# Kernel optimization log

Measured on AMD Instinct MI355X. Metric: run time of the kernel, lower is better.

## Reference

```python
import jax, jax.numpy as jnp
import numpy as np

N_NODES = 50000
N_EDGES = 400000
N_EDGE_SCALARS = 16   # 16x0e block
N_NODE_SCALARS = 64   # 64x0e node attrs
HEADS = 16            # max multiplicity
HEAD_DIM = 32
HID = 64              # mlp_latent_dimensions = [64, 64]
EDGE_DIM = 144        # 16*(1+3+5)
# (start, end, mul, ir.dim) for 16x0e + 16x1o + 16x2e
BLOCKS = [(0, 16, 16, 1), (16, 64, 16, 3), (64, 144, 16, 5)]
ISQRTD = 1.0 / float(np.sqrt(HEAD_DIM))


def _mlp(x, w1, b1, w2, b2, w3, b3):
    # ScalarMLPFunction: Linear -> SiLU -> Linear -> SiLU -> Linear
    h = jax.nn.silu(x @ w1 + b1)
    h = jax.nn.silu(h @ w2 + b2)
    return h @ w3 + b3


def setup_inputs() -> dict:
    key = jax.random.key(0)
    ks = jax.random.split(key, 16)
    def w(k, shape):
        fan_in = shape[0]
        return (jax.random.normal(k, shape, dtype=jnp.float32) / np.sqrt(fan_in)).astype(jnp.float32)
    out_dim = HEADS * HEAD_DIM
    return {
        "edge_index": jax.random.randint(ks[0], (2, N_EDGES), 0, N_NODES, dtype=jnp.int32),
        "edge_feat": jax.random.normal(ks[1], (N_EDGES, EDGE_DIM), dtype=jnp.float32),
        "node_attrs": jax.random.normal(ks[2], (N_NODES, N_NODE_SCALARS), dtype=jnp.float32),
        # node_attr_to_query MLP params
        "q_w1": w(ks[3], (N_NODE_SCALARS, HID)), "q_b1": jnp.zeros((HID,), jnp.float32),
        "q_w2": w(ks[4], (HID, HID)),            "q_b2": jnp.zeros((HID,), jnp.float32),
        "q_w3": w(ks[5], (HID, out_dim)),        "q_b3": jnp.zeros((out_dim,), jnp.float32),
        # edge_feat_to_key MLP params
        "k_w1": w(ks[6], (N_EDGE_SCALARS, HID)), "k_b1": jnp.zeros((HID,), jnp.float32),
        "k_w2": w(ks[7], (HID, HID)),            "k_b2": jnp.zeros((HID,), jnp.float32),
        "k_w3": w(ks[8], (HID, out_dim)),        "k_b3": jnp.zeros((out_dim,), jnp.float32),
    }


def reference(edge_index, edge_feat, node_attrs,
              q_w1, q_b1, q_w2, q_b2, q_w3, q_b3,
              k_w1, k_b1, k_w2, k_b2, k_w3, k_b3):
    edge_center = edge_index[0]  # [E]

    # gather node scalars to edges, then small MLPs -> Q, K per edge
    Q = _mlp(node_attrs[edge_center], q_w1, q_b1, q_w2, q_b2, q_w3, q_b3)
    Q = Q.reshape(-1, HEADS, HEAD_DIM)
    edge_scalars = edge_feat[:, :N_EDGE_SCALARS]
    K = _mlp(edge_scalars, k_w1, k_b1, k_w2, k_b2, k_w3, k_b3)
    K = K.reshape(-1, HEADS, HEAD_DIM)

    # per-edge, per-head logits
    W = jnp.einsum('ehd,ehd->eh', Q, K) * ISQRTD  # [E, H]

    # scatter-softmax over edges sharing the same center node
    seg_max = jax.ops.segment_max(W, edge_center, num_segments=N_NODES)  # [N, H]
    seg_max = jnp.where(jnp.isfinite(seg_max), seg_max, 0.0)
    ex = jnp.exp(W - seg_max[edge_center])
    denom = jax.ops.segment_sum(ex, edge_center, num_segments=N_NODES)
    attn = ex / denom[edge_center]  # [E, H]

    # reweight each irreps block by per-head attention (head h <-> multiplicity channel)
    E = edge_feat.shape[0]
    weighted = []
    for start, end, mul, dim in BLOCKS:
        blk = edge_feat[:, start:end].reshape(E, mul, dim) * attn[:, :mul, None]
        weighted.append(blk.reshape(E, mul * dim))
    w_edge = jnp.concatenate(weighted, axis=-1)  # [E, EDGE_DIM]

    # scatter-sum edges into center nodes
    return jax.ops.segment_sum(w_edge, edge_center, num_segments=N_NODES)  # [N, EDGE_DIM]
```

## Files before the change

### kernel.cpp

```cpp
#include <hip/hip_runtime.h>
#include <hip/hip_bf16.h>

constexpr int N_NODES  = 50000;
constexpr int N_EDGES  = 400000;
constexpr int EDGE_DIM = 144;
constexpr int HEADS    = 16;
constexpr int HEAD_DIM = 32;
constexpr int OUTD     = 512;
constexpr int HID      = 64;
constexpr int NES      = 16;
constexpr int NNS      = 64;
constexpr int SCAN_B   = 512;
constexpr int NSB      = (N_NODES + SCAN_B - 1) / SCAN_B;
constexpr int NPB_A    = 64;
#define ISQRTD 0.17677669529663687f

__device__ __forceinline__ float silu_f(float x) {
    return x / (1.0f + __expf(-x));
}

__device__ __forceinline__ unsigned fenc(float f) {
    unsigned u = __float_as_uint(f);
    return (u & 0x80000000u) ? ~u : (u | 0x80000000u);
}
__device__ __forceinline__ float fdec(unsigned m) {
    unsigned u = (m & 0x80000000u) ? (m ^ 0x80000000u) : ~m;
    return __uint_as_float(u);
}

__device__ __forceinline__ int headOf(int col) {
    return (col < 16) ? col : ((col < 64) ? (col - 16) / 3 : (col - 64) / 5);
}

__device__ __forceinline__ void storeQ(float* p, float v) { *p = v; }
__device__ __forceinline__ void storeQ(__hip_bfloat16* p, float v) { *p = __float2bfloat16(v); }
__device__ __forceinline__ float loadQ(const float* p) { return *p; }
__device__ __forceinline__ float loadQ(const __hip_bfloat16* p) { return __bfloat162float(*p); }

__global__ __launch_bounds__(256) void prep_kernel(
    const float* __restrict__ w1, const float* __restrict__ w2,
    float* __restrict__ w1T, float* __restrict__ w2T) {
    int t = blockIdx.x * 256 + threadIdx.x;
    if (t < NES * HID) {
        int i = t / HID, j = t % HID;
        w1T[j * NES + i] = w1[t];
    }
    if (t < HID * HID) {
        int i = t / HID, j = t % HID;
        w2T[j * HID + i] = w2[t];
    }
}

__global__ __launch_bounds__(256) void mbuild_kernel(
    const float* __restrict__ qw3, const float* __restrict__ qb3,
    const float* __restrict__ kw3, const float* __restrict__ kb3,
    float* __restrict__ M, float* __restrict__ C0,
    float* __restrict__ Mb, float* __restrict__ c1) {
    const int b = blockIdx.x, t = threadIdx.x;
    if (b < 256) {
        const int o  = b * 256 + t;
        const int hl = o & 3, j = (o >> 2) & 63, i = (o >> 8) & 63, hg = o >> 14;
        const int h  = hg * 4 + hl;
        const float* ka = kw3 + (size_t)i * OUTD + h * HEAD_DIM;
        const float* qa = qw3 + (size_t)j * OUTD + h * HEAD_DIM;
        float s = 0.f;
        #pragma unroll
        for (int d = 0; d < HEAD_DIM; ++d) s += ka[d] * qa[d];
        M[o] = s;
    } else if (b < 260) {
        const int o  = (b - 256) * 256 + t;
        const int hl = o & 3, i = (o >> 2) & 63, hg = o >> 8;
        const int h  = hg * 4 + hl;
        float s = 0.f;
        #pragma unroll
        for (int d = 0; d < HEAD_DIM; ++d)
            s += kw3[(size_t)i * OUTD + h * HEAD_DIM + d] * qb3[h * HEAD_DIM + d];
        C0[o] = s;
    } else if (b < 264) {
        const int o = (b - 260) * 256 + t;
        const int h = o >> 6, j = o & 63;
        float s = 0.f;
        #pragma unroll
        for (int d = 0; d < HEAD_DIM; ++d)
            s += kb3[h * HEAD_DIM + d] * qw3[(size_t)j * OUTD + h * HEAD_DIM + d];
        Mb[o] = s;
    } else {
        if (t < HEADS) {
            float s = 0.f;
            #pragma unroll
            for (int d = 0; d < HEAD_DIM; ++d)
                s += kb3[t * HEAD_DIM + d] * qb3[t * HEAD_DIM + d];
            c1[t] = s;
        }
    }
}

__global__ __launch_bounds__(256) void h2q_kernel(
    const float* __restrict__ node_attrs,
    const float* __restrict__ w1, const float* __restrict__ b1,
    const float* __restrict__ w2, const float* __restrict__ b2,
    const float* __restrict__ Mb, const float* __restrict__ c1,
    float* __restrict__ h2buf, float* __restrict__ Sn) {
    __shared__ float xs[4][NNS];
    __shared__ float h1s[4][HID];
    __shared__ float h2s[4][HID];
    __shared__ float Mbs[HEADS][65];
    __shared__ float c1s[HEADS];
    const int t = threadIdx.x, wid = t >> 6, lane = t & 63;
    for (int o = t; o < HEADS * HID; o += 256) Mbs[o >> 6][o & 63] = Mb[o];
    if (t < HEADS) c1s[t] = c1[t];

    const int n = blockIdx.x * 4 + wid;
    const bool act = n < N_NODES;
    xs[wid][lane] = act ? node_attrs[(size_t)n * NNS + lane] : 0.0f;
    __syncthreads();

    float a = b1[lane];
    #pragma unroll
    for (int i = 0; i < NNS; ++i) a += xs[wid][i] * w1[i * HID + lane];
    h1s[wid][lane] = silu_f(a);
    __syncthreads();

    float a2 = b2[lane];
    #pragma unroll
    for (int i = 0; i < HID; ++i) a2 += h1s[wid][i] * w2[i * HID + lane];
    const float h2v = silu_f(a2);
    h2s[wid][lane] = h2v;
    if (act) h2buf[(size_t)n * HID + lane] = h2v;
    __syncthreads();

    const int h = lane & 15, q = lane >> 4;
    float s = 0.f;
    #pragma unroll
    for (int jj = 0; jj < 16; ++jj) s += h2s[wid][q * 16 + jj] * Mbs[h][q * 16 + jj];
    s += __shfl_xor(s, 16);
    s += __shfl_xor(s, 32);
    if (act && lane < HEADS) Sn[(size_t)n * HEADS + lane] = s + c1s[lane];
}

__global__ __launch_bounds__(256) void papply_kernel(
    const float* __restrict__ h2buf, const float* __restrict__ M,
    const float* __restrict__ C0, float* __restrict__ Pn) {
    const int t  = threadIdx.x;
    const int hg = blockIdx.y;

    float Mreg[HID];
    const float* msrc = M + (size_t)hg * 16384 + (t >> 2) * 256 + (t & 3);
    #pragma unroll
    for (int j = 0; j < HID; ++j) Mreg[j] = msrc[j * 4];
    const float c0 = C0[hg * 256 + t];

    __shared__ float h2s[4][HID];
    const int n0 = blockIdx.x * NPB_A;
    #pragma unroll 1
    for (int s4 = 0; s4 < NPB_A / 4; ++s4) {
        const int nb = n0 + s4 * 4;
        const int nl = nb + (t >> 6);
        const float v = (nl < N_NODES) ? h2buf[(size_t)nl * HID + (t & 63)] : 0.f;
        __syncthreads();
        h2s[t >> 6][t & 63] = v;
        __syncthreads();
        #pragma unroll 1
        for (int mm = 0; mm < 4; ++mm) {
            const int n = nb + mm;
            if (n >= N_NODES) break;
            float acc0 = c0, acc1 = 0.f;
            #pragma unroll
            for (int j = 0; j < HID; j += 2) {
                acc0 += h2s[mm][j]     * Mreg[j];
                acc1 += h2s[mm][j + 1] * Mreg[j + 1];
            }
            Pn[(size_t)n * 1024 + hg * 256 + t] = acc0 + acc1;
        }
    }
}

__global__ __launch_bounds__(256) void zero_counts_kernel(int* __restrict__ counts) {
    int t = blockIdx.x * 256 + threadIdx.x;
    if (t < N_NODES) counts[t] = 0;
}
__global__ __launch_bounds__(256) void hist_kernel(const int* __restrict__ center,
                                                   int* __restrict__ counts) {
    int e = blockIdx.x * 256 + threadIdx.x;
    if (e < N_EDGES) atomicAdd(&counts[center[e]], 1);
}
__global__ __launch_bounds__(SCAN_B) void scan1_kernel(
    const int* __restrict__ counts, int* __restrict__ incl, int* __restrict__ blockSums) {
    __shared__ int sm[SCAN_B];
    const int gid = blockIdx.x * SCAN_B + threadIdx.x;
    sm[threadIdx.x] = (gid < N_NODES) ? counts[gid] : 0;
    __syncthreads();
    #pragma unroll 1
    for (int off = 1; off < SCAN_B; off <<= 1) {
        int t = (threadIdx.x >= off) ? sm[threadIdx.x - off] : 0;
        __syncthreads();
        sm[threadIdx.x] += t;
        __syncthreads();
    }
    if (gid < N_NODES) incl[gid] = sm[threadIdx.x];
    if (threadIdx.x == SCAN_B - 1) blockSums[blockIdx.x] = sm[threadIdx.x];
}
__global__ void scan2_kernel(int* __restrict__ blockSums) {
    if (threadIdx.x == 0 && blockIdx.x == 0) {
        int run = 0;
        for (int i = 0; i < NSB; ++i) { int t = blockSums[i]; blockSums[i] = run; run += t; }
    }
}
__global__ __launch_bounds__(SCAN_B) void scan3_kernel(
    const int* __restrict__ counts, const int* __restrict__ incl,
    const int* __restrict__ blockSums, int* __restrict__ rowStart,
    int* __restrict__ cursor) {
    const int gid = blockIdx.x * SCAN_B + threadIdx.x;
    if (gid < N_NODES) {
        const int excl = incl[gid] - counts[gid] + blockSums[blockIdx.x];
        rowStart[gid] = excl;
        cursor[gid]   = excl;
    }
    if (gid == 0) rowStart[N_NODES] = N_EDGES;
}
__global__ __launch_bounds__(256) void fill_kernel(const int* __restrict__ center,
                                                   int* __restrict__ cursor,
                                                   int* __restrict__ edgeList,
                                                   int* __restrict__ nodeOf) {
    int e = blockIdx.x * 256 + threadIdx.x;
    if (e < N_EDGES) {
        const int c = center[e];
        int pos = atomicAdd(&cursor[c], 1);
        edgeList[pos] = e;
        nodeOf[pos]   = c;
    }
}

__global__ __launch_bounds__(256, 2) void wpass5_kernel(
    const int* __restrict__ edgeList, const int* __restrict__ nodeOf,
    const float* __restrict__ edge_feat,
    const float* __restrict__ w1T, const float* __restrict__ b1,
    const float* __restrict__ w2T, const float* __restrict__ b2,
    const float* __restrict__ Pn, const float* __restrict__ Sn,
    float* __restrict__ Wbuf) {
    const int p = blockIdx.x * 256 + threadIdx.x;
    if (p >= N_EDGES) return;
    const int e = edgeList[p];
    const int c = nodeOf[p];

    float x[NES];
    const float4* ef4 = reinterpret_cast<const float4*>(edge_feat + (size_t)e * EDGE_DIM);
    #pragma unroll
    for (int i = 0; i < NES / 4; ++i) {
        float4 t = ef4[i];
        x[4*i+0] = t.x; x[4*i+1] = t.y; x[4*i+2] = t.z; x[4*i+3] = t.w;
    }

    float h1[HID];
    #pragma unroll
    for (int j = 0; j < HID; ++j) {
        float a0 = 0.f, a1 = 0.f, a2 = 0.f, a3 = 0.f;
        const float* wr = w1T + j * NES;
        #pragma unroll
        for (int i = 0; i < NES; i += 4) {
            a0 += x[i + 0] * wr[i + 0];
            a1 += x[i + 1] * wr[i + 1];
            a2 += x[i + 2] * wr[i + 2];
            a3 += x[i + 3] * wr[i + 3];
        }
        h1[j] = silu_f(b1[j] + ((a0 + a1) + (a2 + a3)));
    }

    float wacc[HEADS];
    {
        const float4* s4 = (const float4*)(Sn + (size_t)c * HEADS);
        #pragma unroll
        for (int k = 0; k < 4; ++k) {
            float4 v = s4[k];
            wacc[4*k+0] = v.x; wacc[4*k+1] = v.y; wacc[4*k+2] = v.z; wacc[4*k+3] = v.w;
        }
    }

    const float* prow = Pn + (size_t)c * 1024;
    #pragma unroll 2
    for (int j = 0; j < HID; ++j) {
        float a0 = 0.f, a1 = 0.f, a2 = 0.f, a3 = 0.f;
        const float* wr = w2T + j * HID;
        #pragma unroll
        for (int i = 0; i < HID; i += 4) {
            a0 += h1[i + 0] * wr[i + 0];
            a1 += h1[i + 1] * wr[i + 1];
            a2 += h1[i + 2] * wr[i + 2];
            a3 += h1[i + 3] * wr[i + 3];
        }
        const float h2 = silu_f(b2[j] + ((a0 + a1) + (a2 + a3)));
        #pragma unroll
        for (int hg = 0; hg < 4; ++hg) {
            const float4 pv = *(const float4*)(prow + hg * 256 + j * 4);
            wacc[hg*4+0] += h2 * pv.x;
            wacc[hg*4+1] += h2 * pv.y;
            wacc[hg*4+2] += h2 * pv.z;
            wacc[hg*4+3] += h2 * pv.w;
        }
    }

    float4* wrow = (float4*)(Wbuf + (size_t)p * HEADS);
    #pragma unroll
    for (int k = 0; k < 4; ++k) {
        wrow[k] = make_float4(wacc[4*k+0] * ISQRTD, wacc[4*k+1] * ISQRTD,
                              wacc[4*k+2] * ISQRTD, wacc[4*k+3] * ISQRTD);
    }
}

__global__ __launch_bounds__(256) void gather4_kernel(
    const int* __restrict__ rowStart, const int* __restrict__ edgeList,
    const float* __restrict__ edge_feat, const float* __restrict__ Wbuf,
    float* __restrict__ out) {
    const int wid  = threadIdx.x >> 6;
    const int lane = threadIdx.x & 63;
    const int n = blockIdx.x * 4 + wid;
    if (n >= N_NODES) return;
    const int rs = rowStart[n];
    const int d  = rowStart[n + 1] - rs;

    const int c0 = lane, c1 = lane + 64, c2 = lane + 128;
    const int h0 = headOf(c0);
    const int h1 = headOf(c1);
    const int h2 = (c2 < EDGE_DIM) ? headOf(c2) : 0;
    const bool has2 = (c2 < EDGE_DIM);

    float acc0 = 0.f, acc1 = 0.f, acc2 = 0.f;
    if (d > 0) {
        const int hh  = lane & 15;
        const int sub = lane >> 4;
        float m = -3.0e38f;
        for (int i = sub; i < d; i += 4)
            m = fmaxf(m, Wbuf[(size_t)(rs + i) * HEADS + hh]);
        m = fmaxf(m, __shfl_xor(m, 16));
        m = fmaxf(m, __shfl_xor(m, 32));
        float s = 0.f;
        for (int i = sub; i < d; i += 4)
            s += __expf(Wbuf[(size_t)(rs + i) * HEADS + hh] - m);
        s += __shfl_xor(s, 16);
        s += __shfl_xor(s, 32);
        const float rden = 1.0f / s;

        int i = 0;
        for (; i + 4 <= d; i += 4) {
            const int eA = edgeList[rs + i + 0];
            const int eB = edgeList[rs + i + 1];
            const int eC = edgeList[rs + i + 2];
            const int eD = edgeList[rs + i + 3];
            const float wA = Wbuf[(size_t)(rs + i + 0) * HEADS + hh];
            const float wB = Wbuf[(size_t)(rs + i + 1) * HEADS + hh];
            const float wC = Wbuf[(size_t)(rs + i + 2) * HEADS + hh];
            const float wD = Wbuf[(size_t)(rs + i + 3) * HEADS + hh];
            const float* frA = edge_feat + (size_t)eA * EDGE_DIM;
            const float* frB = edge_feat + (size_t)eB * EDGE_DIM;
            const float* frC = edge_feat + (size_t)eC * EDGE_DIM;
            const float* frD = edge_feat + (size_t)eD * EDGE_DIM;
            const float fA0 = frA[c0], fB0 = frB[c0], fC0 = frC[c0], fD0 = frD[c0];
            const float fA1 = frA[c1], fB1 = frB[c1], fC1 = frC[c1], fD1 = frD[c1];
            const float fA2 = has2 ? frA[c2] : 0.f;
            const float fB2 = has2 ? frB[c2] : 0.f;
            const float fC2 = has2 ? frC[c2] : 0.f;
            const float fD2 = has2 ? frD[c2] : 0.f;

            const float aLA = __expf(wA - m) * rden;
            const float aLB = __expf(wB - m) * rden;
            const float aLC = __expf(wC - m) * rden;
            const float aLD = __expf(wD - m) * rden;
            const float aA0 = __shfl(aLA, h0), aB0 = __shfl(aLB, h0);
            const float aC0 = __shfl(aLC, h0), aD0 = __shfl(aLD, h0);
            const float aA1 = __shfl(aLA, h1), aB1 = __shfl(aLB, h1);
            const float aC1 = __shfl(aLC, h1), aD1 = __shfl(aLD, h1);
            const float aA2 = __shfl(aLA, h2), aB2 = __shfl(aLB, h2);
            const float aC2 = __shfl(aLC, h2), aD2 = __shfl(aLD, h2);

            acc0 += (fA0 * aA0 + fB0 * aB0) + (fC0 * aC0 + fD0 * aD0);
            acc1 += (fA1 * aA1 + fB1 * aB1) + (fC1 * aC1 + fD1 * aD1);
            acc2 += (fA2 * aA2 + fB2 * aB2) + (fC2 * aC2 + fD2 * aD2);
        }
        for (; i < d; ++i) {
            const int eA = edgeList[rs + i];
            const float wA = Wbuf[(size_t)(rs + i) * HEADS + hh];
            const float* frA = edge_feat + (size_t)eA * EDGE_DIM;
            const float aLA = __expf(wA - m) * rden;
            const float aA0 = __shfl(aLA, h0);
            const float aA1 = __shfl(aLA, h1);
            const float aA2 = __shfl(aLA, h2);
            acc0 += frA[c0] * aA0;
            acc1 += frA[c1] * aA1;
            if (has2) acc2 += frA[c2] * aA2;
        }
    }
    float* orow = out + (size_t)n * EDGE_DIM;
    orow[c0] = acc0;
    orow[c1] = acc1;
    if (has2) orow[c2] = acc2;
}

template <typename QT>
__global__ __launch_bounds__(256) void qmlp_kernel(
    const float* __restrict__ node_attrs,
    const float* __restrict__ w1, const float* __restrict__ b1,
    const float* __restrict__ w2, const float* __restrict__ b2,
    const float* __restrict__ w3, const float* __restrict__ b3,
    QT* __restrict__ qn) {
    __shared__ float xs[4][NNS];
    __shared__ float hs[4][HID];
    const int wid  = threadIdx.x >> 6;
    const int lane = threadIdx.x & 63;
    const int node = blockIdx.x * 4 + wid;
    const bool act = node < N_NODES;

    xs[wid][lane] = act ? node_attrs[(size_t)node * NNS + lane] : 0.0f;
    __syncthreads();
    float a = b1[lane];
    #pragma unroll
    for (int i = 0; i < NNS; ++i) a += xs[wid][i] * w1[i * HID + lane];
    a = silu_f(a);
    hs[wid][lane] = a;
    __syncthreads();
    float a2 = b2[lane];
    #pragma unroll
    for (int i = 0; i < HID; ++i) a2 += hs[wid][i] * w2[i * HID + lane];
    a2 = silu_f(a2);
    __syncthreads();
    xs[wid][lane] = a2;
    __syncthreads();
    if (act) {
        #pragma unroll 1
        for (int j8 = 0; j8 < 8; ++j8) {
            const int col = j8 * 64 + lane;
            float acc = b3[col];
            #pragma unroll
            for (int i = 0; i < HID; ++i) acc += xs[wid][i] * w3[i * OUTD + col];
            storeQ(qn + (size_t)node * OUTD + col, acc);
        }
    }
}

__global__ __launch_bounds__(256) void init_kernel(float* __restrict__ out,
                                                   float* __restrict__ denom,
                                                   unsigned* __restrict__ segmax) {
    int t = blockIdx.x * 256 + threadIdx.x;
    if (t < N_NODES * EDGE_DIM) out[t] = 0.0f;
    if (t < N_NODES * HEADS) {
        denom[t]  = 0.0f;
        segmax[t] = 0u;
    }
}

template <typename QT>
__global__ __launch_bounds__(256) void kmlp_kernel(
    const int* __restrict__ center, const float* __restrict__ edge_feat,
    const float* __restrict__ w1, const float* __restrict__ b1,
    const float* __restrict__ w2, const float* __restrict__ b2,
    const float* __restrict__ w3, const float* __restrict__ b3,
    const QT* __restrict__ qn, float* __restrict__ Wbuf,
    unsigned* __restrict__ segmax) {
    const int e = blockIdx.x * 256 + threadIdx.x;
    if (e >= N_EDGES) return;
    const int c = center[e];
    float x[NES];
    const float4* ef4 = reinterpret_cast<const float4*>(edge_feat + (size_t)e * EDGE_DIM);
    #pragma unroll
    for (int i = 0; i < NES / 4; ++i) {
        float4 t = ef4[i];
        x[4*i+0] = t.x; x[4*i+1] = t.y; x[4*i+2] = t.z; x[4*i+3] = t.w;
    }
    float h1[HID];
    #pragma unroll
    for (int j = 0; j < HID; ++j) {
        float a = 0.f;
        #pragma unroll
        for (int i = 0; i < NES; ++i) a += x[i] * w1[i * HID + j];
        h1[j] = silu_f(b1[j] + a);
    }
    float h2[HID];
    #pragma unroll
    for (int j = 0; j < HID; ++j) {
        float a = 0.f;
        #pragma unroll
        for (int i = 0; i < HID; ++i) a += h1[i] * w2[i * HID + j];
        h2[j] = silu_f(b2[j] + a);
    }
    const QT* q = qn + (size_t)c * OUTD;
    #pragma unroll 1
    for (int h = 0; h < HEADS; ++h) {
        float wacc = 0.0f;
        #pragma unroll 1
        for (int jj = 0; jj < HEAD_DIM; ++jj) {
            const int j = h * HEAD_DIM + jj;
            float a = 0.f;
            #pragma unroll
            for (int i = 0; i < HID; ++i) a += h2[i] * w3[i * OUTD + j];
            wacc += (b3[j] + a) * loadQ(q + j);
        }
        const float Wv = wacc * ISQRTD;
        Wbuf[(size_t)e * HEADS + h] = Wv;
        atomicMax(&segmax[c * HEADS + h], fenc(Wv));
    }
}

__global__ __launch_bounds__(256) void ex_denom_kernel(
    const int* __restrict__ center, const unsigned* __restrict__ segmax,
    float* __restrict__ Wbuf, float* __restrict__ denom) {
    const int t = blockIdx.x * 256 + threadIdx.x;
    if (t >= N_EDGES * HEADS) return;
    const int e = t >> 4;
    const int h = t & 15;
    const int c = center[e];
    const float m  = fdec(segmax[c * HEADS + h]);
    const float ex = __expf(Wbuf[t] - m);
    Wbuf[t] = ex;
    atomicAdd(&denom[c * HEADS + h], ex);
}

__global__ __launch_bounds__(256) void attn_kernel(
    const int* __restrict__ center, float* __restrict__ Wbuf,
    const float* __restrict__ denom) {
    const int t = blockIdx.x * 256 + threadIdx.x;
    if (t >= N_EDGES * HEADS) return;
    const int e = t >> 4;
    const int h = t & 15;
    Wbuf[t] = Wbuf[t] / denom[center[e] * HEADS + h];
}

__global__ __launch_bounds__(256) void scatter4_kernel(
    const int* __restrict__ center, const float* __restrict__ edge_feat,
    const float* __restrict__ attn, float* __restrict__ out) {
    const int t = blockIdx.x * 256 + threadIdx.x;
    if (t >= N_EDGES * (EDGE_DIM / 4)) return;
    const int e  = t / (EDGE_DIM / 4);
    const int cg = t - e * (EDGE_DIM / 4);
    const int c  = center[e];
    const float4 f = *(const float4*)(edge_feat + (size_t)e * EDGE_DIM + cg * 4);
    const float* arow = attn + (size_t)e * HEADS;
    const float vals[4] = {f.x, f.y, f.z, f.w};
    #pragma unroll
    for (int k = 0; k < 4; ++k) {
        const int col = cg * 4 + k;
        const int h = headOf(col);
        atomicAdd(out + (size_t)c * EDGE_DIM + col, vals[k] * arow[h]);
    }
}

extern "C" void kernel_launch(void* const* d_in, const int* in_sizes, int n_in,
                              void* d_out, int out_size, void* d_ws, size_t ws_size,
                              hipStream_t stream) {
    const int*   edge_index = (const int*)d_in[0];
    const float* edge_feat  = (const float*)d_in[1];
    const float* node_attrs = (const float*)d_in[2];
    const float* q_w1 = (const float*)d_in[3];
    const float* q_b1 = (const float*)d_in[4];
    const float* q_w2 = (const float*)d_in[5];
    const float* q_b2 = (const float*)d_in[6];
    const float* q_w3 = (const float*)d_in[7];
    const float* q_b3 = (const float*)d_in[8];
    const float* k_w1 = (const float*)d_in[9];
    const float* k_b1 = (const float*)d_in[10];
    const float* k_w2 = (const float*)d_in[11];
    const float* k_b2 = (const float*)d_in[12];
    const float* k_w3 = (const float*)d_in[13];
    const float* k_b3 = (const float*)d_in[14];
    const int* center = edge_index;
    float* out = (float*)d_out;

    const size_t szP   = (size_t)N_NODES * HID * HEADS * sizeof(float);
    const size_t szH2  = (size_t)N_NODES * HID * sizeof(float);
    const size_t szS   = (size_t)N_NODES * HEADS * sizeof(float);
    const size_t szW   = (size_t)N_EDGES * HEADS * sizeof(float);
    const size_t szM   = (size_t)HID * HID * HEADS * sizeof(float);
    const size_t szMisc= (1024 + 1024 + 64 + NES * HID + HID * HID) * sizeof(float);
    const size_t szCSR = ((size_t)4 * N_NODES + N_NODES + 1 + 256 + 2 * N_EDGES) * sizeof(int);

    const int h2qGrid     = (N_NODES + 3) / 4;
    const dim3 papGrid((N_NODES + NPB_A - 1) / NPB_A, 4);
    const int edgeGrid    = (N_EDGES + 255) / 256;
    const int nodeGrid256 = (N_NODES + 255) / 256;
    const int gatherGrid  = (N_NODES + 3) / 4;
    const int ehGrid      = (N_EDGES * HEADS + 255) / 256;

    const size_t need = szP + szH2 + szS + szW + szM + szMisc + szCSR + 4096;

    if (ws_size >= need) {
        char* p = (char*)d_ws;
        float* Pn    = (float*)p;  p += szP;
        float* h2buf = (float*)p;  p += szH2;
        float* Sn    = (float*)p;  p += szS;
        float* Wbuf  = (float*)p;  p += szW;
        float* Mmat  = (float*)p;  p += szM;
        float* C0    = (float*)p;  p += 1024 * sizeof(float);
        float* Mb    = (float*)p;  p += 1024 * sizeof(float);
        float* c1v   = (float*)p;  p += 64 * sizeof(float);
        float* w1T   = (float*)p;  p += NES * HID * sizeof(float);
        float* w2T   = (float*)p;  p += HID * HID * sizeof(float);
        int* counts   = (int*)p;
        int* incl     = counts + N_NODES;
        int* rowStart = incl + N_NODES;
        int* cursor   = rowStart + N_NODES + 1;
        int* blockSums= cursor + N_NODES;
        int* edgeList = blockSums + 256;
        int* nodeOf   = edgeList + N_EDGES;

        prep_kernel<<<16, 256, 0, stream>>>(k_w1, k_w2, w1T, w2T);
        mbuild_kernel<<<265, 256, 0, stream>>>(q_w3, q_b3, k_w3, k_b3, Mmat, C0, Mb, c1v);
        h2q_kernel<<<h2qGrid, 256, 0, stream>>>(
            node_attrs, q_w1, q_b1, q_w2, q_b2, Mb, c1v, h2buf, Sn);
        papply_kernel<<<papGrid, 256, 0, stream>>>(h2buf, Mmat, C0, Pn);

        zero_counts_kernel<<<nodeGrid256, 256, 0, stream>>>(counts);
        hist_kernel<<<edgeGrid, 256, 0, stream>>>(center, counts);
        scan1_kernel<<<NSB, SCAN_B, 0, stream>>>(counts, incl, blockSums);
        scan2_kernel<<<1, 64, 0, stream>>>(blockSums);
        scan3_kernel<<<NSB, SCAN_B, 0, stream>>>(counts, incl, blockSums, rowStart, cursor);
        fill_kernel<<<edgeGrid, 256, 0, stream>>>(center, cursor, edgeList, nodeOf);

        wpass5_kernel<<<edgeGrid, 256, 0, stream>>>(
            edgeList, nodeOf, edge_feat, w1T, k_b1, w2T, k_b2, Pn, Sn, Wbuf);
        gather4_kernel<<<gatherGrid, 256, 0, stream>>>(rowStart, edgeList, edge_feat, Wbuf, out);
        return;
    }

    const size_t szQ   = (size_t)N_NODES * OUTD * sizeof(float);
    char* p = (char*)d_ws;
    float*    Wbuf   = (float*)p;    p += szW;
    float*    denom  = (float*)p;    p += szS;
    unsigned* segmax = (unsigned*)p; p += szS;
    const size_t fbase = (size_t)(p - (char*)d_ws);
    const bool qf32 = ws_size >= fbase + szQ;

    const int initGrid    = (N_NODES * EDGE_DIM + 255) / 256;
    const int scatterGrid = (N_EDGES * (EDGE_DIM / 4) + 255) / 256;
    const int qmlpGrid    = (N_NODES + 3) / 4;

    init_kernel<<<initGrid, 256, 0, stream>>>(out, denom, segmax);
    if (qf32) {
        float* qn = (float*)p;
        qmlp_kernel<float><<<qmlpGrid, 256, 0, stream>>>(
            node_attrs, q_w1, q_b1, q_w2, q_b2, q_w3, q_b3, qn);
        kmlp_kernel<float><<<edgeGrid, 256, 0, stream>>>(
            center, edge_feat, k_w1, k_b1, k_w2, k_b2, k_w3, k_b3, qn, Wbuf, segmax);
    } else {
        __hip_bfloat16* qn = (__hip_bfloat16*)p;
        qmlp_kernel<__hip_bfloat16><<<qmlpGrid, 256, 0, stream>>>(
            node_attrs, q_w1, q_b1, q_w2, q_b2, q_w3, q_b3, qn);
        kmlp_kernel<__hip_bfloat16><<<edgeGrid, 256, 0, stream>>>(
            center, edge_feat, k_w1, k_b1, k_w2, k_b2, k_w3, k_b3, qn, Wbuf, segmax);
    }
    ex_denom_kernel<<<ehGrid, 256, 0, stream>>>(center, segmax, Wbuf, denom);
    attn_kernel<<<ehGrid, 256, 0, stream>>>(center, Wbuf, denom);
    scatter4_kernel<<<scatterGrid, 256, 0, stream>>>(center, edge_feat, Wbuf, out);
}
```

Before: 481.8 us.

## Split per-edge key MLP across two threads with shuffle reduction

Each edge is now handled by a pair of threads. Each thread computes half of the first hidden layer, a partial dot product for the second layer that is combined with a lane shuffle, and 8 of the 16 head accumulators. This cuts registers per thread, removing the 64-float h1 array, so occupancy and parallelism can rise. In exchange it adds a shuffle per hidden unit and duplicates some work, such as the silu on h2 and the loads of edge features, indices and weights.

```diff
diff --git a/kernel.cpp b/kernel.cpp
--- a/kernel.cpp
+++ b/kernel.cpp
@@ -231,31 +231,38 @@
     }
 }
 
-__global__ __launch_bounds__(256, 2) void wpass5_kernel(
+__global__ __launch_bounds__(256) void wpass8_kernel(
     const int* __restrict__ edgeList, const int* __restrict__ nodeOf,
     const float* __restrict__ edge_feat,
     const float* __restrict__ w1T, const float* __restrict__ b1,
     const float* __restrict__ w2T, const float* __restrict__ b2,
     const float* __restrict__ Pn, const float* __restrict__ Sn,
     float* __restrict__ Wbuf) {
-    const int p = blockIdx.x * 256 + threadIdx.x;
-    if (p >= N_EDGES) return;
-    const int e = edgeList[p];
-    const int c = nodeOf[p];
+    const int t    = threadIdx.x;
+    const int half = t & 1;
+    const int el   = t >> 1;
+    const int slot = blockIdx.x * 128 + el;
+    const bool act = slot < N_EDGES;
+
+    int e = 0, c = 0;
+    if (act) { e = edgeList[slot]; c = nodeOf[slot]; }
 
     float x[NES];
-    const float4* ef4 = reinterpret_cast<const float4*>(edge_feat + (size_t)e * EDGE_DIM);
-    #pragma unroll
-    for (int i = 0; i < NES / 4; ++i) {
-        float4 t = ef4[i];
-        x[4*i+0] = t.x; x[4*i+1] = t.y; x[4*i+2] = t.z; x[4*i+3] = t.w;
-    }
-
-    float h1[HID];
-    #pragma unroll
-    for (int j = 0; j < HID; ++j) {
+    {
+        const float4* ef4 = reinterpret_cast<const float4*>(edge_feat + (size_t)e * EDGE_DIM);
+        #pragma unroll
+        for (int i = 0; i < NES / 4; ++i) {
+            float4 v = act ? ef4[i] : make_float4(0.f, 0.f, 0.f, 0.f);
+            x[4*i+0] = v.x; x[4*i+1] = v.y; x[4*i+2] = v.z; x[4*i+3] = v.w;
+        }
+    }
+
+    float h1r[32];
+    #pragma unroll
+    for (int jj = 0; jj < 32; ++jj) {
+        const int j = half * 32 + jj;
+        const float* wr = w1T + j * NES;
         float a0 = 0.f, a1 = 0.f, a2 = 0.f, a3 = 0.f;
-        const float* wr = w1T + j * NES;
         #pragma unroll
         for (int i = 0; i < NES; i += 4) {
             a0 += x[i + 0] * wr[i + 0];
@@ -263,47 +270,46 @@
             a2 += x[i + 2] * wr[i + 2];
             a3 += x[i + 3] * wr[i + 3];
         }
-        h1[j] = silu_f(b1[j] + ((a0 + a1) + (a2 + a3)));
-    }
-
-    float wacc[HEADS];
+        h1r[jj] = silu_f(b1[j] + ((a0 + a1) + (a2 + a3)));
+    }
+
+    float wacc[8];
     {
-        const float4* s4 = (const float4*)(Sn + (size_t)c * HEADS);
-        #pragma unroll
-        for (int k = 0; k < 4; ++k) {
-            float4 v = s4[k];
-            wacc[4*k+0] = v.x; wacc[4*k+1] = v.y; wacc[4*k+2] = v.z; wacc[4*k+3] = v.w;
-        }
-    }
-
-    const float* prow = Pn + (size_t)c * 1024;
-    #pragma unroll 2
+        const float4* s4 = (const float4*)(Sn + (size_t)c * HEADS + half * 8);
+        const float4 v0 = s4[0], v1 = s4[1];
+        wacc[0] = v0.x; wacc[1] = v0.y; wacc[2] = v0.z; wacc[3] = v0.w;
+        wacc[4] = v1.x; wacc[5] = v1.y; wacc[6] = v1.z; wacc[7] = v1.w;
+    }
+
+    const float* ph = Pn + (size_t)c * 1024 + (half * 2) * 256;
+    #pragma unroll 4
     for (int j = 0; j < HID; ++j) {
+        const float* wr = w2T + j * HID + half * 32;
         float a0 = 0.f, a1 = 0.f, a2 = 0.f, a3 = 0.f;
-        const float* wr = w2T + j * HID;
-        #pragma unroll
-        for (int i = 0; i < HID; i += 4) {
-            a0 += h1[i + 0] * wr[i + 0];
-            a1 += h1[i + 1] * wr[i + 1];
-            a2 += h1[i + 2] * wr[i + 2];
-            a3 += h1[i + 3] * wr[i + 3];
-        }
-        const float h2 = silu_f(b2[j] + ((a0 + a1) + (a2 + a3)));
-        #pragma unroll
-        for (int hg = 0; hg < 4; ++hg) {
-            const float4 pv = *(const float4*)(prow + hg * 256 + j * 4);
-            wacc[hg*4+0] += h2 * pv.x;
-            wacc[hg*4+1] += h2 * pv.y;
-            wacc[hg*4+2] += h2 * pv.z;
-            wacc[hg*4+3] += h2 * pv.w;
-        }
-    }
-
-    float4* wrow = (float4*)(Wbuf + (size_t)p * HEADS);
-    #pragma unroll
-    for (int k = 0; k < 4; ++k) {
-        wrow[k] = make_float4(wacc[4*k+0] * ISQRTD, wacc[4*k+1] * ISQRTD,
-                              wacc[4*k+2] * ISQRTD, wacc[4*k+3] * ISQRTD);
+        #pragma unroll
+        for (int i = 0; i < 32; i += 4) {
+            a0 += h1r[i + 0] * wr[i + 0];
+            a1 += h1r[i + 1] * wr[i + 1];
+            a2 += h1r[i + 2] * wr[i + 2];
+            a3 += h1r[i + 3] * wr[i + 3];
+        }
+        float part = (a0 + a1) + (a2 + a3);
+        part += __shfl_xor(part, 1);
+        const float h2 = silu_f(b2[j] + part);
+        const float4 p0 = *(const float4*)(ph + j * 4);
+        const float4 p1 = *(const float4*)(ph + 256 + j * 4);
+        wacc[0] += h2 * p0.x; wacc[1] += h2 * p0.y;
+        wacc[2] += h2 * p0.z; wacc[3] += h2 * p0.w;
+        wacc[4] += h2 * p1.x; wacc[5] += h2 * p1.y;
+        wacc[6] += h2 * p1.z; wacc[7] += h2 * p1.w;
+    }
+
+    if (act) {
+        float4* wrow = (float4*)(Wbuf + (size_t)slot * HEADS + half * 8);
+        wrow[0] = make_float4(wacc[0] * ISQRTD, wacc[1] * ISQRTD,
+                              wacc[2] * ISQRTD, wacc[3] * ISQRTD);
+        wrow[1] = make_float4(wacc[4] * ISQRTD, wacc[5] * ISQRTD,
+                              wacc[6] * ISQRTD, wacc[7] * ISQRTD);
     }
 }
 
@@ -574,6 +580,7 @@
     const int h2qGrid     = (N_NODES + 3) / 4;
     const dim3 papGrid((N_NODES + NPB_A - 1) / NPB_A, 4);
     const int edgeGrid    = (N_EDGES + 255) / 256;
+    const int wpassGrid   = (N_EDGES + 127) / 128;
     const int nodeGrid256 = (N_NODES + 255) / 256;
     const int gatherGrid  = (N_NODES + 3) / 4;
     const int ehGrid      = (N_EDGES * HEADS + 255) / 256;
@@ -613,7 +620,7 @@
         scan3_kernel<<<NSB, SCAN_B, 0, stream>>>(counts, incl, blockSums, rowStart, cursor);
         fill_kernel<<<edgeGrid, 256, 0, stream>>>(center, cursor, edgeList, nodeOf);
 
-        wpass5_kernel<<<edgeGrid, 256, 0, stream>>>(
+        wpass8_kernel<<<wpassGrid, 256, 0, stream>>>(
             edgeList, nodeOf, edge_feat, w1T, k_b1, w2T, k_b2, Pn, Sn, Wbuf);
         gather4_kernel<<<gatherGrid, 256, 0, stream>>>(rowStart, edgeList, edge_feat, Wbuf, out);
         return;
```

After: 901.4 us. 1.87x slower.
